# Performance work log

Hardware: AMD Instinct MI355X
Metric: run time of the kernel (lower is better)

The kernel has to match this reference:

```python
import jax, jax.numpy as jnp
import numpy as np
from jax import lax

C = 64
K = 3
RED = 8


def _lrelu(x):
    return jax.nn.leaky_relu(x, 0.1)


def setup_inputs() -> dict:
    key = jax.random.key(0)
    ks = jax.random.split(key, 8)
    b, h, w = 32, 128, 128
    x0 = jax.random.normal(ks[0], (b, C, h, w), dtype=jnp.float32)
    v = jax.random.normal(ks[1], (b, C), dtype=jnp.float32)
    s = 0.05
    # CA layer: two 1x1 convs (no bias) acting on the [b,64] embedding
    ca_w1 = jax.random.normal(ks[2], (C // RED, C), dtype=jnp.float32) * s
    ca_w2 = jax.random.normal(ks[3], (C, C // RED), dtype=jnp.float32) * s
    # kernel-generating MLP: Linear(64,64) -> LeakyReLU -> Linear(64, 64*K*K), no bias
    k_w1 = jax.random.normal(ks[4], (C, C), dtype=jnp.float32) * s
    k_w2 = jax.random.normal(ks[5], (C * K * K, C), dtype=jnp.float32) * s
    # final 1x1 conv (default_conv, bias=True)
    conv_w = jax.random.normal(ks[6], (C, C), dtype=jnp.float32) * s
    conv_b = jax.random.normal(ks[7], (C,), dtype=jnp.float32) * s
    return {"x0": x0, "v": v, "ca_w1": ca_w1, "ca_w2": ca_w2,
            "k_w1": k_w1, "k_w2": k_w2, "conv_w": conv_w, "conv_b": conv_b}


def reference(x0, v, ca_w1, ca_w2, k_w1, k_w2, conv_w, conv_b):
    b, c, h, w = x0.shape
    # Channel attention: sigmoid(W2 @ lrelu(W1 @ v)) gates x0 per (b,c)
    att = jax.nn.sigmoid(_lrelu(v @ ca_w1.T) @ ca_w2.T)  # [b, c]
    out = x0 * att[:, :, None, None]
    # Per-sample, per-channel K x K kernels generated from the embedding
    kern = (_lrelu(v @ k_w1.T) @ k_w2.T).reshape(b * c, 1, K, K)
    p = (K - 1) // 2
    y = lax.conv_general_dilated(
        out.reshape(1, b * c, h, w), kern,
        window_strides=(1, 1), padding=[(p, p), (p, p)],
        feature_group_count=b * c,
        dimension_numbers=("NCHW", "OIHW", "NCHW"))
    y = _lrelu(y).reshape(b, c, h, w)
    # final 1x1 conv with bias
    return jnp.einsum("bchw,oc->bohw", y, conv_w) + conv_b[None, :, None, None]
```

## Files before the change

kernel.cpp:

```cpp
#include <hip/hip_runtime.h>

#define HW 128
#define XBb 16
#define XBf 4
#define KTb 24592
#define LDS_BYTES 27664

typedef __attribute__((ext_vector_type(8))) short  bfrag;
typedef __attribute__((ext_vector_type(16))) float f16x;
typedef __attribute__((ext_vector_type(4)))  float f4;

__device__ __forceinline__ float lrelu(float x) { return x > 0.f ? x : 0.1f * x; }

__device__ __forceinline__ short f2bf(float f) {
    unsigned u = __builtin_bit_cast(unsigned, f);
    u = u + 0x7FFFu + ((u >> 16) & 1u);
    return (short)(u >> 16);
}

__device__ float g_ktab[32 * 768];
__device__ short g_whi[4096];

__global__ __launch_bounds__(64) void dgfem_prep(
    const float* __restrict__ v, const float* __restrict__ ca_w1,
    const float* __restrict__ ca_w2, const float* __restrict__ k_w1,
    const float* __restrict__ k_w2, const float* __restrict__ conv_w)
{
    const int b = blockIdx.x;
    const int t = threadIdx.x;

    if (b == 32) {
        for (int i = t; i < 4096; i += 64) g_whi[i] = f2bf(conv_w[i]);
        return;
    }

    __shared__ float vb[64], t1[8], att[64], t2[64];
    vb[t] = v[b * 64 + t];
    __syncthreads();

    if (t < 8) {
        float s = 0.f;
        for (int j = 0; j < 64; ++j) s += vb[j] * ca_w1[t * 64 + j];
        t1[t] = lrelu(s);
    }
    {
        float s = 0.f;
        for (int j = 0; j < 64; ++j) s += vb[j] * k_w1[t * 64 + j];
        t2[t] = lrelu(s);
    }
    __syncthreads();
    {
        float s = 0.f;
        for (int i = 0; i < 8; ++i) s += t1[i] * ca_w2[t * 8 + i];
        att[t] = 1.f / (1.f + expf(-s));
    }
    __syncthreads();
    for (int r = t; r < 576; r += 64) {
        int c = r / 9, tp = r - c * 9;
        float s = 0.f;
        for (int j = 0; j < 64; ++j) s += t2[j] * k_w2[r * 64 + j];
        int m = c >> 4, g = (c >> 3) & 1, a = (c >> 2) & 1, j2 = c & 3;
        g_ktab[b * 768 + (((m * 2 + a) * 2 + g) * 4 + j2) * 12 + tp] = s * att[c];
    }
}

__global__ __launch_bounds__(256)
__attribute__((amdgpu_waves_per_eu(8)))
void dgfem_main(
    const float* __restrict__ x0, const float* __restrict__ conv_b,
    float* __restrict__ out)
{
    const int t  = threadIdx.x;
    const int w  = t >> 6;
    const int l  = t & 63;
    const int g  = l >> 5;
    const int ln = l & 31;
    const int px = w * 32 + ln;

    const int bid  = blockIdx.x;
    const int orig = (bid & 7) * 512 + (bid >> 3);
    const int b    = orig >> 7;
    const int gy   = orig & 127;

    __shared__ __align__(16) char lds[LDS_BYTES];
    float* ldsf = (float*)lds;

    {
        const float* ksrc = g_ktab + b * 768;
        const float rm0 = (gy > 0)   ? 1.f : 0.f;
        const float rm2 = (gy < 127) ? 1.f : 0.f;
        for (int i = t; i < 768; i += 256) {
            int tp = i % 12;
            float val = (tp < 9) ? ksrc[i] : 0.f;
            float rm = (tp < 3) ? rm0 : ((tp < 6) ? 1.f : rm2);
            *(float*)(lds + KTb + i * 4) = val * rm;
        }
    }

    const int doff = w * 1024 + l * 16;
    int inv0, inv1, inv2;
    {
        #pragma unroll
        for (int q = 0; q < 3; ++q) {
            int F      = q * 4096 + doff;
            int slot   = F / 1536;
            int within = F - slot * 1536;
            int rowq   = gy - 1 + (within >> 9);
            int crow   = min(max(rowq, 0), 127);
            int gs = slot >> 2, j2s = slot & 3;
            int iv = (gs * 8 + j2s) * 65536 + crow * 512 + (within & 511);
            if (q == 0) inv0 = iv; else if (q == 1) inv1 = iv; else inv2 = iv;
        }
    }

    const char* xb = (const char*)x0 + ((size_t)b << 22);

    #define STAGE(rr_, sel_)                                                   \
    {                                                                          \
        const char* srcb = xb + ((size_t)(((rr_) >> 1) * 16 + ((rr_) & 1) * 4) << 16); \
        char* dstb = lds + XBb + (sel_) * 12288 + doff;                        \
        __builtin_amdgcn_global_load_lds(                                      \
            (const __attribute__((address_space(1))) unsigned*)(srcb + inv0),  \
            (__attribute__((address_space(3))) unsigned*)(dstb), 16, 0, 0);    \
        __builtin_amdgcn_global_load_lds(                                      \
            (const __attribute__((address_space(1))) unsigned*)(srcb + inv1),  \
            (__attribute__((address_space(3))) unsigned*)(dstb + 4096), 16, 0, 0); \
        __builtin_amdgcn_global_load_lds(                                      \
            (const __attribute__((address_space(1))) unsigned*)(srcb + inv2),  \
            (__attribute__((address_space(3))) unsigned*)(dstb + 8192), 16, 0, 0); \
    }

    f16x acc0, acc1;
    #pragma unroll
    for (int i = 0; i < 16; ++i) { acc0[i] = 0.f; acc1[i] = 0.f; }

    const float mLf = (px > 0)   ? 1.f : 0.f;
    const float mRf = (px < 127) ? 1.f : 0.f;

    bfrag yh;

    STAGE(0, 0);
    __syncthreads();

    #define ROUND(rr_, a_, m_, sel_)                                           \
    {                                                                          \
        if ((rr_) < 7) STAGE((rr_) + 1, (sel_) ^ 1);                           \
        const float* xbase = ldsf + (XBf + (sel_) * 3072 + g * 1536 + px - 1); \
        const char*  kb = lds + KTb + ((rr_) * 8 + g * 4) * 48;                \
        _Pragma("unroll")                                                      \
        for (int j2 = 0; j2 < 4; ++j2) {                                       \
            const f4* kf = (const f4*)(kb + j2 * 48);                          \
            f4 kA = kf[0], kB = kf[1], kC = kf[2];                             \
            const float* bA = xbase + j2 * 384;                                \
            float xL0 = bA[0]   * mLf, xC0 = bA[1],   xR0 = bA[2]   * mRf;     \
            float xL1 = bA[128] * mLf, xC1 = bA[129], xR1 = bA[130] * mRf;     \
            float xL2 = bA[256] * mLf, xC2 = bA[257], xR2 = bA[258] * mRf;     \
            float aY = fmaf(kA.x, xL0, fmaf(kA.y, xC0, kA.z * xR0))            \
                     + fmaf(kA.w, xL1, fmaf(kB.x, xC1, kB.y * xR1))            \
                     + fmaf(kB.z, xL2, fmaf(kB.w, xC2, kC.x * xR2));           \
            yh[(a_) * 4 + j2] = f2bf(lrelu(aY));                               \
        }                                                                      \
        if (a_) {                                                              \
            const char* whb = (const char*)g_whi + ln * 128 + g * 16 + (m_) * 32; \
            bfrag whi0 = *(const bfrag*)(whb);                                 \
            bfrag whi1 = *(const bfrag*)(whb + 4096);                          \
            acc0 = __builtin_amdgcn_mfma_f32_32x32x16_bf16(whi0, yh, acc0, 0, 0, 0); \
            acc1 = __builtin_amdgcn_mfma_f32_32x32x16_bf16(whi1, yh, acc1, 0, 0, 0); \
        }                                                                      \
        if ((rr_) < 7) __syncthreads();                                        \
    }

    ROUND(0, 0, 0, 0);
    ROUND(1, 1, 0, 1);
    ROUND(2, 0, 1, 0);
    ROUND(3, 1, 1, 1);
    ROUND(4, 0, 2, 0);
    ROUND(5, 1, 2, 1);
    ROUND(6, 0, 3, 0);
    ROUND(7, 1, 3, 1);

    #undef ROUND
    #undef STAGE

    float* ob = out + ((size_t)b << 20) + (size_t)gy * HW + px;
    #pragma unroll
    for (int q = 0; q < 4; ++q) {
        const int obase = 8 * q + 4 * g;
        float4 bv0 = *(const float4*)&conv_b[obase];
        float4 bv1 = *(const float4*)&conv_b[32 + obase];
        const float* b0f = (const float*)&bv0;
        const float* b1f = (const float*)&bv1;
        #pragma unroll
        for (int r2 = 0; r2 < 4; ++r2) {
            ob[(size_t)(obase + r2) * 16384]      = acc0[q * 4 + r2] + b0f[r2];
            ob[(size_t)(32 + obase + r2) * 16384] = acc1[q * 4 + r2] + b1f[r2];
        }
    }
}

extern "C" void kernel_launch(void* const* d_in, const int* in_sizes, int n_in,
                              void* d_out, int out_size, void* d_ws, size_t ws_size,
                              hipStream_t stream) {
    const float* x0     = (const float*)d_in[0];
    const float* v      = (const float*)d_in[1];
    const float* ca_w1  = (const float*)d_in[2];
    const float* ca_w2  = (const float*)d_in[3];
    const float* k_w1   = (const float*)d_in[4];
    const float* k_w2   = (const float*)d_in[5];
    const float* conv_w = (const float*)d_in[6];
    const float* conv_b = (const float*)d_in[7];
    float* outp = (float*)d_out;

    dgfem_prep<<<dim3(33), dim3(64), 0, stream>>>(v, ca_w1, ca_w2, k_w1, k_w2, conv_w);
    dgfem_main<<<dim3(4096), dim3(256), 0, stream>>>(x0, conv_b, outp);
}
```

Before: 80.09 us.

## Load input rows directly from global memory and stage only bf16 conv outputs in LDS

```diff
diff --git a/kernel.cpp b/kernel.cpp
--- a/kernel.cpp
+++ b/kernel.cpp
@@ -1,10 +1,8 @@
 #include <hip/hip_runtime.h>
 
 #define HW 128
-#define XBb 16
-#define XBf 4
-#define KTb 24592
-#define LDS_BYTES 27664
+#define YBb 3072
+#define LDS_BYTES 7168
 
 typedef __attribute__((ext_vector_type(8))) short  bfrag;
 typedef __attribute__((ext_vector_type(16))) float f16x;
@@ -16,6 +14,10 @@
     unsigned u = __builtin_bit_cast(unsigned, f);
     u = u + 0x7FFFu + ((u >> 16) & 1u);
     return (short)(u >> 16);
+}
+__device__ __forceinline__ unsigned rne_u(float f) {
+    unsigned u = __builtin_bit_cast(unsigned, f);
+    return u + 0x7FFFu + ((u >> 16) & 1u);
 }
 
 __device__ float g_ktab[32 * 768];
@@ -59,8 +61,7 @@
         int c = r / 9, tp = r - c * 9;
         float s = 0.f;
         for (int j = 0; j < 64; ++j) s += t2[j] * k_w2[r * 64 + j];
-        int m = c >> 4, g = (c >> 3) & 1, a = (c >> 2) & 1, j2 = c & 3;
-        g_ktab[b * 768 + (((m * 2 + a) * 2 + g) * 4 + j2) * 12 + tp] = s * att[c];
+        g_ktab[b * 768 + c * 12 + tp] = s * att[c];
     }
 }
 
@@ -70,12 +71,12 @@
     const float* __restrict__ x0, const float* __restrict__ conv_b,
     float* __restrict__ out)
 {
-    const int t  = threadIdx.x;
-    const int w  = t >> 6;
-    const int l  = t & 63;
-    const int g  = l >> 5;
-    const int ln = l & 31;
-    const int px = w * 32 + ln;
+    const int t   = threadIdx.x;
+    const int w   = t >> 6, l = t & 63;
+    const int g   = l >> 5, ln = l & 31;
+    const int px  = w * 32 + ln;
+    const int pxg = t & 31, j = t >> 5;
+    const int px0 = pxg << 2;
 
     const int bid  = blockIdx.x;
     const int orig = (bid & 7) * 512 + (bid >> 3);
@@ -93,94 +94,88 @@
             int tp = i % 12;
             float val = (tp < 9) ? ksrc[i] : 0.f;
             float rm = (tp < 3) ? rm0 : ((tp < 6) ? 1.f : rm2);
-            *(float*)(lds + KTb + i * 4) = val * rm;
+            ldsf[i] = val * rm;
         }
     }
 
-    const int doff = w * 1024 + l * 16;
-    int inv0, inv1, inv2;
-    {
-        #pragma unroll
-        for (int q = 0; q < 3; ++q) {
-            int F      = q * 4096 + doff;
-            int slot   = F / 1536;
-            int within = F - slot * 1536;
-            int rowq   = gy - 1 + (within >> 9);
-            int crow   = min(max(rowq, 0), 127);
-            int gs = slot >> 2, j2s = slot & 3;
-            int iv = (gs * 8 + j2s) * 65536 + crow * 512 + (within & 511);
-            if (q == 0) inv0 = iv; else if (q == 1) inv1 = iv; else inv2 = iv;
-        }
-    }
-
-    const char* xb = (const char*)x0 + ((size_t)b << 22);
-
-    #define STAGE(rr_, sel_)                                                   \
-    {                                                                          \
-        const char* srcb = xb + ((size_t)(((rr_) >> 1) * 16 + ((rr_) & 1) * 4) << 16); \
-        char* dstb = lds + XBb + (sel_) * 12288 + doff;                        \
-        __builtin_amdgcn_global_load_lds(                                      \
-            (const __attribute__((address_space(1))) unsigned*)(srcb + inv0),  \
-            (__attribute__((address_space(3))) unsigned*)(dstb), 16, 0, 0);    \
-        __builtin_amdgcn_global_load_lds(                                      \
-            (const __attribute__((address_space(1))) unsigned*)(srcb + inv1),  \
-            (__attribute__((address_space(3))) unsigned*)(dstb + 4096), 16, 0, 0); \
-        __builtin_amdgcn_global_load_lds(                                      \
-            (const __attribute__((address_space(1))) unsigned*)(srcb + inv2),  \
-            (__attribute__((address_space(3))) unsigned*)(dstb + 8192), 16, 0, 0); \
-    }
+    const float mL = (pxg > 0)  ? 1.f : 0.f;
+    const float mR = (pxg < 31) ? 1.f : 0.f;
+    const int   dL = (pxg > 0)  ? -4 : 0;
+    const int   dR = (pxg < 31) ? 16 : 0;
+    int preQ[3];
+    {
+        int r0 = max(gy - 1, 0), r1 = gy, r2 = min(gy + 1, 127);
+        preQ[0] = (j << 16) + r0 * 512 + px0 * 4;
+        preQ[1] = (j << 16) + r1 * 512 + px0 * 4;
+        preQ[2] = (j << 16) + r2 * 512 + px0 * 4;
+    }
+    const char* xbu   = (const char*)x0 + ((size_t)b << 22);
+    const int   kaddr = j * 48;
 
     f16x acc0, acc1;
     #pragma unroll
     for (int i = 0; i < 16; ++i) { acc0[i] = 0.f; acc1[i] = 0.f; }
 
-    const float mLf = (px > 0)   ? 1.f : 0.f;
-    const float mRf = (px < 127) ? 1.f : 0.f;
-
-    bfrag yh;
-
-    STAGE(0, 0);
-    __syncthreads();
-
-    #define ROUND(rr_, a_, m_, sel_)                                           \
+    __syncthreads();
+
+    #define ROUND(rr_, a_, m_)                                                 \
     {                                                                          \
-        if ((rr_) < 7) STAGE((rr_) + 1, (sel_) ^ 1);                           \
-        const float* xbase = ldsf + (XBf + (sel_) * 3072 + g * 1536 + px - 1); \
-        const char*  kb = lds + KTb + ((rr_) * 8 + g * 4) * 48;                \
+                     \
+        float a0 = 0.f, a1 = 0.f, a2 = 0.f, a3 = 0.f;                          \
+        const char* kbp = lds + kaddr + (rr_) * 384;                           \
+        f4 kf0 = *(const f4*)(kbp);                                            \
+        f4 kf1 = *(const f4*)(kbp + 16);                                       \
+        float k8v = *(const float*)(kbp + 32);                                 \
         _Pragma("unroll")                                                      \
-        for (int j2 = 0; j2 < 4; ++j2) {                                       \
-            const f4* kf = (const f4*)(kb + j2 * 48);                          \
-            f4 kA = kf[0], kB = kf[1], kC = kf[2];                             \
-            const float* bA = xbase + j2 * 384;                                \
-            float xL0 = bA[0]   * mLf, xC0 = bA[1],   xR0 = bA[2]   * mRf;     \
-            float xL1 = bA[128] * mLf, xC1 = bA[129], xR1 = bA[130] * mRf;     \
-            float xL2 = bA[256] * mLf, xC2 = bA[257], xR2 = bA[258] * mRf;     \
-            float aY = fmaf(kA.x, xL0, fmaf(kA.y, xC0, kA.z * xR0))            \
-                     + fmaf(kA.w, xL1, fmaf(kB.x, xC1, kB.y * xR1))            \
-                     + fmaf(kB.z, xL2, fmaf(kB.w, xC2, kC.x * xR2));           \
-            yh[(a_) * 4 + j2] = f2bf(lrelu(aY));                               \
+        for (int r = 0; r < 3; ++r) {                                          \
+            const unsigned oQ = ((unsigned)(rr_) << 19) + (unsigned)preQ[r];   \
+            f4    Q = *(const f4*)(xbu + oQ);                                  \
+            float L = *(const float*)(xbu + oQ + dL);                          \
+            float R = *(const float*)(xbu + oQ + dR);                          \
+            float k0, k1, k2;                                                  \
+            if (r == 0)      { k0 = kf0.x; k1 = kf0.y; k2 = kf0.z; }           \
+            else if (r == 1) { k0 = kf0.w; k1 = kf1.x; k2 = kf1.y; }           \
+            else             { k0 = kf1.z; k1 = kf1.w; k2 = k8v;   }           \
+            float Lm = L * mL, Rm = R * mR;                                    \
+            a0 += fmaf(k0, Lm,  fmaf(k1, Q.x, k2 * Q.y));                      \
+            a1 += fmaf(k0, Q.x, fmaf(k1, Q.y, k2 * Q.z));                      \
+            a2 += fmaf(k0, Q.y, fmaf(k1, Q.z, k2 * Q.w));                      \
+            a3 += fmaf(k0, Q.z, fmaf(k1, Q.w, k2 * Rm));                       \
         }                                                                      \
+        unsigned u0 = rne_u(lrelu(a0)), u1 = rne_u(lrelu(a1));                 \
+        unsigned u2 = rne_u(lrelu(a2)), u3 = rne_u(lrelu(a3));                 \
+        uint2 pk;                                                              \
+        pk.x = (u0 >> 16) | (u1 & 0xFFFF0000u);                                \
+        pk.y = (u2 >> 16) | (u3 & 0xFFFF0000u);                                \
+        *(uint2*)(lds + YBb + ((a_) * 8 + j) * 256 + pxg * 8) = pk;            \
         if (a_) {                                                              \
+            asm volatile("s_waitcnt lgkmcnt(0)" ::: "memory");                 \
+            __builtin_amdgcn_s_barrier();                                      \
+            __builtin_amdgcn_sched_barrier(0);                                 \
+            bfrag yh;                                                          \
+            const char* yrb = lds + YBb + g * 2048 + px * 2;                   \
+            _Pragma("unroll")                                                  \
+            for (int jj = 0; jj < 8; ++jj)                                     \
+                yh[jj] = *(const short*)(yrb + jj * 256);                      \
             const char* whb = (const char*)g_whi + ln * 128 + g * 16 + (m_) * 32; \
             bfrag whi0 = *(const bfrag*)(whb);                                 \
             bfrag whi1 = *(const bfrag*)(whb + 4096);                          \
             acc0 = __builtin_amdgcn_mfma_f32_32x32x16_bf16(whi0, yh, acc0, 0, 0, 0); \
             acc1 = __builtin_amdgcn_mfma_f32_32x32x16_bf16(whi1, yh, acc1, 0, 0, 0); \
+            if ((m_) < 3) __syncthreads();    \
         }                                                                      \
-        if ((rr_) < 7) __syncthreads();                                        \
-    }
-
-    ROUND(0, 0, 0, 0);
-    ROUND(1, 1, 0, 1);
-    ROUND(2, 0, 1, 0);
-    ROUND(3, 1, 1, 1);
-    ROUND(4, 0, 2, 0);
-    ROUND(5, 1, 2, 1);
-    ROUND(6, 0, 3, 0);
-    ROUND(7, 1, 3, 1);
+    }
+
+    ROUND(0, 0, 0);
+    ROUND(1, 1, 0);
+    ROUND(2, 0, 1);
+    ROUND(3, 1, 1);
+    ROUND(4, 0, 2);
+    ROUND(5, 1, 2);
+    ROUND(6, 0, 3);
+    ROUND(7, 1, 3);
 
     #undef ROUND
-    #undef STAGE
 
     float* ob = out + ((size_t)b << 20) + (size_t)gy * HW + px;
     #pragma unroll
```

Measured after the change: 233.1 us. 2.91x slower.
